# Kernel optimization log

Hardware: AMD Instinct MI355X
Metric: run time of the kernel (lower is better)

The kernel has to match this reference:

```python
import jax, jax.numpy as jnp
import numpy as np

HIDDEN_DIM = 4096
MM_DIM = 7


def setup_inputs() -> dict:
    key = jax.random.key(0)
    k_img, k_a = jax.random.split(key)
    images = jax.random.normal(k_img, (64, 576, MM_DIM), dtype=jnp.float32)
    # Fixed orthogonal buffer A, as in load_model: QR of a random gaussian matrix.
    rm = np.asarray(jax.random.normal(k_a, (HIDDEN_DIM, HIDDEN_DIM), dtype=jnp.float32))
    Q, _ = np.linalg.qr(rm.astype(np.float64), mode='complete')
    A = jnp.asarray(Q.astype(np.float32))
    return {"images": images, "A": A}


def reference(images, A):
    # Original: F.pad(x, (0, hidden_dim - mm_dim)) @ A.
    # Zero-padded columns contribute nothing, so this is exactly
    # x @ A[:mm_dim, :]  (a [*, 7] x [7, 4096] contraction).
    return jnp.einsum('btm,mh->bth', images, A[:MM_DIM, :])
```

## Files before the change

kernel.cpp:

```cpp
#include <hip/hip_runtime.h>


typedef float f4 __attribute__((ext_vector_type(4)));

#define NROWS (64 * 576)
#define HID   4096
#define MM    7
#define RPB   8

__global__ __launch_bounds__(256) void vt_kernel(const float* __restrict__ images,
                                                 const float* __restrict__ A,
                                                 float* __restrict__ out) {
    const int row0 = blockIdx.x * RPB;

    float x[RPB][MM];
#pragma unroll
    for (int r = 0; r < RPB; ++r) {
#pragma unroll
        for (int m = 0; m < MM; ++m) {
            x[r][m] = images[(size_t)(row0 + r) * MM + m];
        }
    }

#pragma unroll
    for (int it = 0; it < 4; ++it) {
        const int h = (threadIdx.x << 2) + (it << 10);

        f4 a[MM];
#pragma unroll
        for (int m = 0; m < MM; ++m) {
            a[m] = *(const f4*)(A + (size_t)m * HID + h);
        }

#pragma unroll
        for (int r = 0; r < RPB; ++r) {
            f4 acc = x[r][0] * a[0];
#pragma unroll
            for (int m = 1; m < MM; ++m) {
                acc += x[r][m] * a[m];
            }
            __builtin_nontemporal_store(acc, (f4*)(out + (size_t)(row0 + r) * HID + h));
        }
    }
}

extern "C" void kernel_launch(void* const* d_in, const int* in_sizes, int n_in,
                              void* d_out, int out_size, void* d_ws, size_t ws_size,
                              hipStream_t stream) {
    const float* images = (const float*)d_in[0];
    const float* A      = (const float*)d_in[1];
    float* out          = (float*)d_out;

    const int nblocks = NROWS / RPB;
    vt_kernel<<<nblocks, 256, 0, stream>>>(images, A, out);
}
```

Measured before the change: 610.6 us.

## Keep A slice in registers and process more rows per block

Each thread now loads its whole 7x16 slice of A into registers once, then loops over 18 rows per block in groups of 6, writing every output row fully. The grid shrinks to 2048 blocks, and a launch bound with a minimum of 3 blocks per SM is added. Non-temporal stores are replaced with plain stores. The aim is to cut redundant A loads and block launch overhead in this store-bound kernel. The cost is higher register pressure, fewer blocks in flight, and possible cache pollution from the plain stores.

```diff
diff --git a/kernel.cpp b/kernel.cpp
--- a/kernel.cpp
+++ b/kernel.cpp
@@ -3,43 +3,53 @@
 
 typedef float f4 __attribute__((ext_vector_type(4)));
 
-#define NROWS (64 * 576)
-#define HID   4096
-#define MM    7
-#define RPB   8
+#define NROWS  (64 * 576)
+#define HID    4096
+#define MM     7
+#define NW     4
+#define BLOCKS 2048
+#define RPB    18
+#define SUB    6
 
-__global__ __launch_bounds__(256) void vt_kernel(const float* __restrict__ images,
-                                                 const float* __restrict__ A,
-                                                 float* __restrict__ out) {
+__global__ __launch_bounds__(256, 3) void vt_kernel(const float* __restrict__ images,
+                                                    const float* __restrict__ A,
+                                                    float* __restrict__ out) {
+    const int tid  = threadIdx.x;
     const int row0 = blockIdx.x * RPB;
 
-    float x[RPB][MM];
+    f4 a[NW][MM];
 #pragma unroll
-    for (int r = 0; r < RPB; ++r) {
+    for (int it = 0; it < NW; ++it) {
 #pragma unroll
         for (int m = 0; m < MM; ++m) {
-            x[r][m] = images[(size_t)(row0 + r) * MM + m];
+            a[it][m] = *(const f4*)(A + (size_t)m * HID + (it << 10) + (tid << 2));
         }
     }
 
+    for (int g = 0; g < RPB / SUB; ++g) {
+        const int r0 = row0 + g * SUB;
+
+        float x[SUB][MM];
 #pragma unroll
-    for (int it = 0; it < 4; ++it) {
-        const int h = (threadIdx.x << 2) + (it << 10);
-
-        f4 a[MM];
+        for (int r = 0; r < SUB; ++r) {
 #pragma unroll
-        for (int m = 0; m < MM; ++m) {
-            a[m] = *(const f4*)(A + (size_t)m * HID + h);
+            for (int m = 0; m < MM; ++m) {
+                x[r][m] = images[(size_t)(r0 + r) * MM + m];
+            }
         }
 
 #pragma unroll
-        for (int r = 0; r < RPB; ++r) {
-            f4 acc = x[r][0] * a[0];
+        for (int r = 0; r < SUB; ++r) {
+            float* orow = out + (size_t)(r0 + r) * HID + (tid << 2);
 #pragma unroll
-            for (int m = 1; m < MM; ++m) {
-                acc += x[r][m] * a[m];
+            for (int it = 0; it < NW; ++it) {
+                f4 acc = x[r][0] * a[it][0];
+#pragma unroll
+                for (int m = 1; m < MM; ++m) {
+                    acc += x[r][m] * a[it][m];
+                }
+                *(f4*)(orow + (it << 10)) = acc;
             }
-            __builtin_nontemporal_store(acc, (f4*)(out + (size_t)(row0 + r) * HID + h));
         }
     }
 }
@@ -51,6 +61,5 @@
     const float* A      = (const float*)d_in[1];
     float* out          = (float*)d_out;
 
-    const int nblocks = NROWS / RPB;
-    vt_kernel<<<nblocks, 256, 0, stream>>>(images, A, out);
+    vt_kernel<<<BLOCKS, 256, 0, stream>>>(images, A, out);
 }
```

Result: no change. 622.7 us (+2.0%).
